# Kernel tuning notes

Hardware: AMD Instinct MI355X
Metric: run time of the kernel (lower is better)

## Reference

```python
import jax, jax.numpy as jnp
import numpy as np

# dims (match init_kwargs)
T, B, N, D_OB = 256, 32, 64, 4
D_MODEL = N * D_OB            # 256
D_PE = 16
D_T = D_MODEL + D_PE          # 272 transformer width
H = 8
DH = D_T // H                 # 34
L = 2
DFF = 1024
C = 2
MAX_LEN = T
F_IN = T * D_OB               # 1024, ObservationPropagation channels


def setup_inputs() -> dict:
    key = jax.random.key(0)
    ks = jax.random.split(key, 24)
    g = lambda k, shp: 0.02 * jax.random.normal(k, shp, dtype=jnp.float32)
    return {
        "x": jax.random.normal(ks[0], (T, B, N), dtype=jnp.float32),
        "times": jnp.sort(jax.random.uniform(ks[1], (T, B), dtype=jnp.float32) * MAX_LEN, axis=0),
        "lengths": jax.random.randint(ks[2], (B,), MAX_LEN // 2, MAX_LEN + 1),
        "R_u": g(ks[3], (1, N * D_OB)),
        "Wv1": g(ks[4], (F_IN, F_IN)), "bv1": g(ks[5], (F_IN,)),
        "Wv2": g(ks[6], (F_IN, F_IN)), "bv2": g(ks[7], (F_IN,)),
        "qkv_w": g(ks[8], (L, D_T, 3 * D_T)), "qkv_b": g(ks[9], (L, 3 * D_T)),
        "out_w": g(ks[10], (L, D_T, D_T)), "out_b": g(ks[11], (L, D_T)),
        "ln1_w": jnp.ones((L, D_T), jnp.float32), "ln1_b": jnp.zeros((L, D_T), jnp.float32),
        "ln2_w": jnp.ones((L, D_T), jnp.float32), "ln2_b": jnp.zeros((L, D_T), jnp.float32),
        "ffn_w1": g(ks[12], (L, D_T, DFF)), "ffn_b1": g(ks[13], (L, DFF)),
        "ffn_w2": g(ks[14], (L, DFF, D_T)), "ffn_b2": g(ks[15], (L, D_T)),
        "mlp_w1": g(ks[16], (D_T, D_T)), "mlp_b1": g(ks[17], (D_T,)),
        "mlp_w2": g(ks[18], (D_T, C)), "mlp_b2": g(ks[19], (C,)),
    }


def _pos_encode(times):
    # PositionalEncodingTF: timescales = max_len ** linspace(0,1,d_pe//2)
    scales = MAX_LEN ** np.linspace(0.0, 1.0, D_PE // 2)
    st = times[..., None] / jnp.asarray(scales, times.dtype)  # [T,B,8]
    return jnp.concatenate([jnp.sin(st), jnp.cos(st)], axis=-1)  # [T,B,16]


def _segment_softmax(w, seg, num_segments):
    m = jax.ops.segment_max(w, seg, num_segments=num_segments)
    e = jnp.exp(w - m[seg])
    s = jax.ops.segment_sum(e, seg, num_segments=num_segments)
    return e / s[seg]


def _ob_propagate(xn, src, tgt, edge_w, Wv, bv):
    """Batched ObservationPropagation (use_beta=False, decompose=False).
    xn: [B,N,F]; messages = relu(lin_value(x_src)) * softmax(edge_w per target);
    scatter-add at targets. Returns (out, pre-softmax alpha == edge_w)."""
    gamma = _segment_softmax(edge_w, tgt, N)              # [E]
    value = jax.nn.relu(xn @ Wv + bv)                     # [B,N,F] (linear commutes with gather)
    msg = value[:, src, :] * gamma[None, :, None]         # [B,E,F] -- dominant memory traffic
    out = jnp.zeros_like(xn).at[:, tgt, :].add(msg)       # segment-sum at target nodes
    return out, edge_w


def _ln(x, w, b):
    mu = jnp.mean(x, axis=-1, keepdims=True)
    var = jnp.mean((x - mu) ** 2, axis=-1, keepdims=True)
    return (x - mu) / jnp.sqrt(var + 1e-5) * w + b


def _encoder_layer(xt, key_pad, qkv_w, qkv_b, out_w, out_b, ln1_w, ln1_b, ln2_w, ln2_b, w1, b1, w2, b2):
    # xt: [T,B,D_T]; key_pad: [B,T] True = padded. Post-norm torch TransformerEncoderLayer, relu, no dropout.
    Tt, Bb, _ = xt.shape
    q, k, v = jnp.split(xt @ qkv_w + qkv_b, 3, axis=-1)
    to_h = lambda t: t.reshape(Tt, Bb, H, DH).transpose(1, 2, 0, 3)  # [B,H,T,dh]
    scores = jnp.einsum("bhqd,bhkd->bhqk", to_h(q), to_h(k)) / jnp.sqrt(jnp.asarray(DH, xt.dtype))
    scores = jnp.where(key_pad[:, None, None, :], -jnp.inf, scores)
    attn = jax.nn.softmax(scores, axis=-1)
    o = jnp.einsum("bhqk,bhkd->bhqd", attn, to_h(v)).transpose(2, 0, 1, 3).reshape(Tt, Bb, D_T)
    xt = _ln(xt + o @ out_w + out_b, ln1_w, ln1_b)
    ff = jax.nn.relu(xt @ w1 + b1) @ w2 + b2
    return _ln(xt + ff, ln2_w, ln2_b)


def _forward(x, times, lengths, R_u, Wv1, bv1, Wv2, bv2, qkv_w, qkv_b, out_w, out_b,
             ln1_w, ln1_b, ln2_w, ln2_b, ffn_w1, ffn_b1, ffn_w2, ffn_b2,
             mlp_w1, mlp_b1, mlp_w2, mlp_b2):
    Bb = x.shape[1]
    # observation embedding: repeat each sensor d_ob times, scale by R_u, relu
    h = jax.nn.relu(jnp.repeat(x, D_OB, axis=-1) * R_u)          # [T,B,N*d_ob]
    pe = _pos_encode(times)                                      # [T,B,16]
    key_pad = jnp.arange(T)[None, :] >= lengths[:, None]         # [B,T]
    # reshape to per-sensor node features: [B, N, T*d_ob]
    xn = h.reshape(T, Bb, N, D_OB).transpose(1, 2, 0, 3).reshape(Bb, N, F_IN)
    # dense all-pairs graph (global_structure = ones); torch.nonzero order is row-major
    src = jnp.repeat(jnp.arange(N), N)   # edge_index[0]
    tgt = jnp.tile(jnp.arange(N), N)     # edge_index[1] (aggregation index)
    ew = jnp.ones((N * N,), x.dtype)
    xn, ew2 = _ob_propagate(xn, src, tgt, ew, Wv1, bv1)
    xn, _ = _ob_propagate(xn, src, tgt, ew2, Wv2, bv2)
    out = xn.reshape(Bb, N, T, D_OB).transpose(2, 0, 1, 3).reshape(T, Bb, N * D_OB)
    out = jnp.concatenate([out, pe], axis=2)                     # [T,B,272]
    for l in range(L):
        out = _encoder_layer(out, key_pad, qkv_w[l], qkv_b[l], out_w[l], out_b[l],
                             ln1_w[l], ln1_b[l], ln2_w[l], ln2_b[l],
                             ffn_w1[l], ffn_b1[l], ffn_w2[l], ffn_b2[l])
    keep = (~key_pad).T[:, :, None].astype(out.dtype)            # [T,B,1]
    agg = jnp.sum(out * keep, axis=0) / (lengths[:, None].astype(out.dtype) + 1.0)
    hid = jax.nn.relu(agg @ mlp_w1 + mlp_b1)
    logits = hid @ mlp_w2 + mlp_b2
    return jax.nn.softmax(logits, axis=1)                        # [B,C]


def reference(x, times, lengths, R_u, Wv1, bv1, Wv2, bv2, qkv_w, qkv_b, out_w, out_b,
              ln1_w, ln1_b, ln2_w, ln2_b, ffn_w1, ffn_b1, ffn_w2, ffn_b2,
              mlp_w1, mlp_b1, mlp_w2, mlp_b2):
    return _forward(x, times, lengths, R_u, Wv1, bv1, Wv2, bv2, qkv_w, qkv_b, out_w, out_b,
                    ln1_w, ln1_b, ln2_w, ln2_b, ffn_w1, ffn_b1, ffn_w2, ffn_b2,
                    mlp_w1, mlp_b1, mlp_w2, mlp_b2)
```

## Files before the change

kernel.cpp:

```cpp
#include <hip/hip_runtime.h>
#include <math.h>

#define T_DIM 256
#define B_DIM 32
#define N_DIM 64
#define F_INF 1024
#define D_T 272
#define D_TP 288
#define H_DIM 8
#define DH_DIM 34
#define DFF_DIM 1024

typedef unsigned int uint;
typedef short bf16x8 __attribute__((ext_vector_type(8)));
typedef float f32x4 __attribute__((ext_vector_type(4)));

__device__ __forceinline__ ushort f2bf(float f) {
    uint u = __float_as_uint(f);
    uint r = (u + 0x7fffu + ((u >> 16) & 1u)) >> 16;
    return (ushort)r;
}
__device__ __forceinline__ float bf2f(ushort u) {
    return __uint_as_float(((uint)u) << 16);
}

__global__ void xn_kernel(const float* __restrict__ x, const float* __restrict__ Ru,
                          ushort* __restrict__ xn) {
    int idx = blockIdx.x * blockDim.x + threadIdx.x;
    if (idx >= B_DIM * N_DIM * F_INF) return;
    int f = idx & 1023;
    int bn = idx >> 10;
    int n = bn & 63;
    int b = bn >> 6;
    int t = f >> 2;
    int d = f & 3;
    float v = x[(t * B_DIM + b) * N_DIM + n] * Ru[(n << 2) + d];
    xn[idx] = f2bf(fmaxf(v, 0.0f));
}

struct WT {
    int tstart[11];
    const float* src[10];
    ushort* dst[10];
    int K[10];
    int N[10];
    int Kp[10];
    int ntn[10];
};
__global__ __launch_bounds__(256) void wconv_tiled(WT s) {
    int tile = blockIdx.x;
    int seg = 0;
    while (seg < 9 && tile >= s.tstart[seg + 1]) ++seg;
    int ti = tile - s.tstart[seg];
    int ntn = s.ntn[seg];
    int tk = ti / ntn, tn = ti - tk * ntn;
    int N = s.N[seg], Kp = s.Kp[seg];
    __shared__ float t[16][17];
    int ty = threadIdx.x >> 4, tx = threadIdx.x & 15;
    t[ty][tx] = s.src[seg][(size_t)(tk * 16 + ty) * N + tn * 16 + tx];
    __syncthreads();
    s.dst[seg][(size_t)(tn * 16 + ty) * Kp + tk * 16 + tx] = f2bf(t[tx][ty]);
}

template <int ACT, int OUT_MODE>
__global__ __launch_bounds__(256) void gemm_mfma(const ushort* __restrict__ A,
                                                 const ushort* __restrict__ Bt,
                                                 const float* __restrict__ bias,
                                                 void* __restrict__ Cout,
                                                 int M, int N, int K, int Kstride) {
    __shared__ ushort As[3][64 * 32];
    __shared__ ushort Bs[3][128 * 32];
    const int tid = threadIdx.x;
    const int m0 = (OUT_MODE == 3) ? 0 : blockIdx.y * 64;
    const int n0 = blockIdx.x * 128;
    if (OUT_MODE == 3) {
        A += (size_t)blockIdx.y * K;
        Bt += (size_t)blockIdx.y * K;
    }
    const int w = tid >> 6, lane = tid & 63;
    const int wr = w >> 1, wc = w & 1;
    const int lr = lane & 15, lk = lane >> 4;

    const int ns = K >> 5;

    const int ra = w * 16 + (lane >> 2);
    const int ca = (((lane & 3) ^ ((ra >> 1) & 3)) << 3);
    int gma = m0 + ra; if (gma > M - 1) gma = M - 1;
    const ushort* gA = &A[(size_t)gma * Kstride + ca];
    const int rb0 = w * 32 + (lane >> 2);
    const int cb0 = (((lane & 3) ^ ((rb0 >> 1) & 3)) << 3);
    const int rb1 = rb0 + 16;
    const int cb1 = (((lane & 3) ^ ((rb1 >> 1) & 3)) << 3);
    int gnb0 = n0 + rb0; if (gnb0 > N - 1) gnb0 = N - 1;
    int gnb1 = n0 + rb1; if (gnb1 > N - 1) gnb1 = N - 1;
    const ushort* gB0 = &Bt[(size_t)gnb0 * Kstride + cb0];
    const ushort* gB1 = &Bt[(size_t)gnb1 * Kstride + cb1];

    f32x4 acc[2][4];
#pragma unroll
    for (int i = 0; i < 2; ++i)
#pragma unroll
        for (int j = 0; j < 4; ++j) acc[i][j] = (f32x4){0.f, 0.f, 0.f, 0.f};

    auto stage = [&](int buf, int s) {
        const int k0 = s << 5;
        __builtin_amdgcn_global_load_lds(
            (const __attribute__((address_space(1))) void*)(gA + k0),
            (__attribute__((address_space(3))) void*)(&As[buf][w * 512]), 16, 0, 0);
        __builtin_amdgcn_global_load_lds(
            (const __attribute__((address_space(1))) void*)(gB0 + k0),
            (__attribute__((address_space(3))) void*)(&Bs[buf][w * 1024]), 16, 0, 0);
        __builtin_amdgcn_global_load_lds(
            (const __attribute__((address_space(1))) void*)(gB1 + k0),
            (__attribute__((address_space(3))) void*)(&Bs[buf][w * 1024 + 512]), 16, 0, 0);
    };

    stage(0, 0);
    stage(1, 1);
    asm volatile("s_waitcnt vmcnt(3)" ::: "memory");
    __builtin_amdgcn_sched_barrier(0);
    __builtin_amdgcn_s_barrier();
    __builtin_amdgcn_sched_barrier(0);

    int cur = 0;
    for (int s = 0; s < ns; ++s) {
        int stg = cur + 2; if (stg >= 3) stg -= 3;
        if (s + 2 < ns) stage(stg, s + 2);

        bf16x8 af[2], bf[4];
#pragma unroll
        for (int mt = 0; mt < 2; ++mt) {
            int row = wr * 32 + mt * 16 + lr;
            int ch = lk ^ ((row >> 1) & 3);
            af[mt] = *reinterpret_cast<const bf16x8*>(&As[cur][row * 32 + ch * 8]);
        }
#pragma unroll
        for (int nt = 0; nt < 4; ++nt) {
            int row = wc * 64 + nt * 16 + lr;
            int ch = lk ^ ((row >> 1) & 3);
            bf[nt] = *reinterpret_cast<const bf16x8*>(&Bs[cur][row * 32 + ch * 8]);
        }
        __builtin_amdgcn_s_setprio(1);
#pragma unroll
        for (int mt = 0; mt < 2; ++mt)
#pragma unroll
            for (int nt = 0; nt < 4; ++nt)
                acc[mt][nt] = __builtin_amdgcn_mfma_f32_16x16x32_bf16(
                    af[mt], bf[nt], acc[mt][nt], 0, 0, 0);
        __builtin_amdgcn_s_setprio(0);

        if (s + 1 < ns) {
            if (s + 2 < ns)
                asm volatile("s_waitcnt vmcnt(3)" ::: "memory");
            else
                asm volatile("s_waitcnt vmcnt(0)" ::: "memory");
            __builtin_amdgcn_sched_barrier(0);
            __builtin_amdgcn_s_barrier();
            __builtin_amdgcn_sched_barrier(0);
        }
        cur = (cur == 2) ? 0 : cur + 1;
    }

    if (OUT_MODE == 4) {
        __shared__ float red[2][128];
        float part[4];
#pragma unroll
        for (int nt = 0; nt < 4; ++nt) {
            int col = n0 + wc * 64 + nt * 16 + lr;
            float bv = bias[col];
            float s = 0.f;
#pragma unroll
            for (int mt = 0; mt < 2; ++mt)
#pragma unroll
                for (int r = 0; r < 4; ++r) s += fmaxf(acc[mt][nt][r] + bv, 0.f);
            s += __shfl_xor(s, 16);
            s += __shfl_xor(s, 32);
            part[nt] = s;
        }
        if (lk == 0) {
#pragma unroll
            for (int nt = 0; nt < 4; ++nt) red[wr][wc * 64 + nt * 16 + lr] = part[nt];
        }
        __syncthreads();
        if (tid < 128) {
            float tot = red[0][tid] + red[1][tid];
            ((ushort*)Cout)[(size_t)blockIdx.y * 1024 + n0 + tid] =
                f2bf(tot * (1.0f / 64.0f));
        }
        return;
    }

#pragma unroll
    for (int nt = 0; nt < 4; ++nt) {
        int col = n0 + wc * 64 + nt * 16 + lr;
        if (col >= N) continue;
        float bv = (OUT_MODE == 3) ? 0.f : bias[col];
        int g = 0, dcol = 0;
        if (OUT_MODE == 2) { g = col / 34; dcol = col - g * 34; }
#pragma unroll
        for (int mt = 0; mt < 2; ++mt) {
#pragma unroll
            for (int r = 0; r < 4; ++r) {
                int row = m0 + wr * 32 + mt * 16 + lk * 4 + r;
                if (row >= M) continue;
                float v = acc[mt][nt][r] + bv;
                if (ACT == 1) v = fmaxf(v, 0.0f);
                if (OUT_MODE == 0)
                    ((float*)Cout)[(size_t)row * N + col] = v;
                else if (OUT_MODE == 1)
                    ((ushort*)Cout)[(size_t)row * N + col] = f2bf(v);
                else if (OUT_MODE == 2)
                    ((ushort*)Cout)[(size_t)row * 960 + g * 40 + dcol] = f2bf(v);
                else
                    ((float*)Cout)[(size_t)(blockIdx.y * M + row) * N + col] = v;
            }
        }
    }
}

__global__ __launch_bounds__(256) void gemm_ln(const ushort* __restrict__ A,
                                               const ushort* __restrict__ Bt,
                                               const float* __restrict__ bias,
                                               const ushort* __restrict__ resid,
                                               const float* __restrict__ lnw,
                                               const float* __restrict__ lnb,
                                               ushort* __restrict__ Out,
                                               int K, int Kstride) {
    __shared__ ushort lds[21504];
    const int tid = threadIdx.x;
    const int m0 = blockIdx.x * 64;
    const int w = tid >> 6, lane = tid & 63;
    const int lr = lane & 15, lk = lane >> 4;
    const int ns = K >> 5;

    const int ra = w * 16 + (lane >> 2);
    const int ca = (((lane & 3) ^ ((ra >> 1) & 3)) << 3);
    const ushort* gA = &A[(size_t)(m0 + ra) * Kstride + ca];

    f32x4 acc[17];
#pragma unroll
    for (int t = 0; t < 17; ++t) acc[t] = (f32x4){0.f, 0.f, 0.f, 0.f};

    auto stage = [&](int buf, int s) {
        const int k0 = s << 5;
        __builtin_amdgcn_global_load_lds(
            (const __attribute__((address_space(1))) void*)(gA + k0),
            (__attribute__((address_space(3))) void*)(&lds[buf * 2048 + w * 512]),
            16, 0, 0);
        for (int c = w; c < 17; c += 4) {
            int row16 = c * 16 + (lane >> 2);
            int p8 = (((lane & 3) ^ ((row16 >> 1) & 3)) << 3);
            const ushort* src = &Bt[(size_t)row16 * Kstride + k0 + p8];
            __builtin_amdgcn_global_load_lds(
                (const __attribute__((address_space(1))) void*)src,
                (__attribute__((address_space(3))) void*)(&lds[4096 + buf * 8704 + c * 512]),
                16, 0, 0);
        }
    };

    stage(0, 0);
    asm volatile("s_waitcnt vmcnt(0)" ::: "memory");
    __builtin_amdgcn_sched_barrier(0);
    __builtin_amdgcn_s_barrier();
    __builtin_amdgcn_sched_barrier(0);

    int cur = 0;
    for (int s = 0; s < ns; ++s) {
        if (s + 1 < ns) stage(cur ^ 1, s + 1);

        bf16x8 af;
        {
            int row = w * 16 + lr;
            int ch = lk ^ ((row >> 1) & 3);
            af = *reinterpret_cast<const bf16x8*>(&lds[cur * 2048 + row * 32 + ch * 8]);
        }
        __builtin_amdgcn_s_setprio(1);
#pragma unroll
        for (int t = 0; t < 17; ++t) {
            int row = t * 16 + lr;
            int ch = lk ^ ((row >> 1) & 3);
            bf16x8 bf = *reinterpret_cast<const bf16x8*>(
                &lds[4096 + cur * 8704 + row * 32 + ch * 8]);
            acc[t] = __builtin_amdgcn_mfma_f32_16x16x32_bf16(af, bf, acc[t], 0, 0, 0);
        }
        __builtin_amdgcn_s_setprio(0);

        if (s + 1 < ns) {
            asm volatile("s_waitcnt vmcnt(0)" ::: "memory");
            __builtin_amdgcn_sched_barrier(0);
            __builtin_amdgcn_s_barrier();
            __builtin_amdgcn_sched_barrier(0);
        }
        cur ^= 1;
    }

    __syncthreads();
    for (int i = tid; i < 64 * 34; i += 256) {
        int row = i / 34, c8 = i - row * 34;
        *reinterpret_cast<uint4*>(&lds[row * 272 + c8 * 8]) =
            *reinterpret_cast<const uint4*>(&resid[(size_t)(m0 + row) * D_TP + c8 * 8]);
    }
    __syncthreads();

    float sum[4] = {0.f, 0.f, 0.f, 0.f}, sq[4] = {0.f, 0.f, 0.f, 0.f};
#pragma unroll
    for (int t = 0; t < 17; ++t) {
        int col = t * 16 + lr;
        float bv = bias[col];
#pragma unroll
        for (int r = 0; r < 4; ++r) {
            int row = w * 16 + lk * 4 + r;
            float v = acc[t][r] + bv + bf2f(lds[row * 272 + col]);
            acc[t][r] = v;
            sum[r] += v;
            sq[r] += v * v;
        }
    }
#pragma unroll
    for (int mask = 1; mask <= 8; mask <<= 1)
#pragma unroll
        for (int r = 0; r < 4; ++r) {
            sum[r] += __shfl_xor(sum[r], mask);
            sq[r] += __shfl_xor(sq[r], mask);
        }
    float mu[4], inv[4];
#pragma unroll
    for (int r = 0; r < 4; ++r) {
        mu[r] = sum[r] * (1.0f / D_T);
        float var = sq[r] * (1.0f / D_T) - mu[r] * mu[r];
        inv[r] = 1.0f / sqrtf(var + 1e-5f);
    }
#pragma unroll
    for (int t = 0; t < 17; ++t) {
        int col = t * 16 + lr;
        float wv = lnw[col], bb = lnb[col];
#pragma unroll
        for (int r = 0; r < 4; ++r) {
            int row = m0 + w * 16 + lk * 4 + r;
            Out[(size_t)row * D_TP + col] = f2bf((acc[t][r] - mu[r]) * inv[r] * wv + bb);
        }
    }
}

__global__ __launch_bounds__(256) void reduce_p2_kernel(const float* __restrict__ part,
                                                        const float* __restrict__ bv2,
                                                        float* __restrict__ out2) {
    int idx = blockIdx.x * 256 + threadIdx.x;
    if (idx >= B_DIM * F_INF) return;
    int g = idx & 1023;
    float s = bv2[g];
#pragma unroll
    for (int ks = 0; ks < 4; ++ks) s += part[(size_t)ks * B_DIM * F_INF + idx];
    out2[idx] = fmaxf(s, 0.f);
}

__global__ void seq_kernel(const float* __restrict__ out2, const float* __restrict__ times,
                           ushort* __restrict__ seq) {
    int idx = blockIdx.x * blockDim.x + threadIdx.x;
    if (idx >= T_DIM * B_DIM * D_TP) return;
    int c = idx % D_TP;
    int tb = idx / D_TP;
    float v;
    if (c < 256) {
        v = out2[(tb % B_DIM) * 1024 + ((tb / B_DIM) << 2) + (c & 3)];
    } else if (c < 272) {
        int s = c - 256;
        int sc = (s < 8) ? s : s - 8;
        float arg = times[tb] * exp2f(-8.0f * (float)sc * (1.0f / 7.0f));
        v = (s < 8) ? sinf(arg) : cosf(arg);
    } else {
        v = 0.f;
    }
    seq[idx] = f2bf(v);
}

struct PadPtrs {
    uint* wt[6];
    int nrows[6];
};
__global__ void init_pads_kernel(uint* __restrict__ qkvb, uint* __restrict__ x1,
                                 uint* __restrict__ attno, PadPtrs p) {
    const int TB = T_DIM * B_DIM;
    int idx = blockIdx.x * blockDim.x + threadIdx.x;
    if (idx < TB * 8) {
        int row = idx >> 3, q = idx & 7;
        x1[(size_t)row * 144 + 136 + q] = 0;
        attno[(size_t)row * 144 + 136 + q] = 0;
        return;
    }
    idx -= TB * 8;
    if (idx < TB * 72) {
        int row = idx / 72;
        int r = idx - row * 72;
        int g = r / 3, q = r - g * 3;
        qkvb[(size_t)row * 480 + g * 20 + 17 + q] = 0;
        return;
    }
    idx -= TB * 72;
#pragma unroll
    for (int sgi = 0; sgi < 6; ++sgi) {
        int cnt = p.nrows[sgi] * 8;
        if (idx < cnt) {
            int row = idx >> 3, q = idx & 7;
            p.wt[sgi][(size_t)row * 144 + 136 + q] = 0;
            return;
        }
        idx -= cnt;
    }
}

__global__ __launch_bounds__(256) void attn_mfma(const ushort* __restrict__ qkv,
                                                 const int* __restrict__ lengths,
                                                 ushort* __restrict__ attno) {
    const int b = blockIdx.x >> 3;
    const int h = blockIdx.x & 7;
    const int tid = threadIdx.x;
    const int w = tid >> 6, lane = tid & 63;
    const int lr = lane & 15, lk = lane >> 4;
    __shared__ ushort Ks[2][64 * 40];
    __shared__ ushort Vt[2][48 * 72];
    __shared__ ushort Ps[4][64 * 72];
    const int len = lengths[b];
    const float scale = 0.1714985851f;
    const bf16x8 zv = {0, 0, 0, 0, 0, 0, 0, 0};

    for (int i = tid; i < 2 * 8 * 72; i += 256) {
        int bb = i / 576;
        Vt[bb][40 * 72 + (i - bb * 576)] = 0;
    }

    const int srow0 = tid / 5, sch0 = tid - srow0 * 5;
    const int srow1 = (tid + 256) / 5, sch1 = (tid + 256) - srow1 * 5;
    const int sjp0 = (srow0 & 15) * 4 + (srow0 >> 4);
    const int sjp1 = (srow1 & 15) * 4 + (srow1 >> 4);
    const bool has1 = (tid < 64);
    bf16x8 kreg0, kreg1, vreg0, vreg1;

    auto LOADS = [&](int c) {
        const ushort* b0 = &qkv[(size_t)((c * 64 + srow0) * 32 + b) * 960 + h * 40];
        kreg0 = *reinterpret_cast<const bf16x8*>(b0 + 320 + sch0 * 8);
        vreg0 = *reinterpret_cast<const bf16x8*>(b0 + 640 + sch0 * 8);
        if (has1) {
            const ushort* b1 = &qkv[(size_t)((c * 64 + srow1) * 32 + b) * 960 + h * 40];
            kreg1 = *reinterpret_cast<const bf16x8*>(b1 + 320 + sch1 * 8);
            vreg1 = *reinterpret_cast<const bf16x8*>(b1 + 640 + sch1 * 8);
        }
    };
    auto WRITES = [&](int buf) {
        *reinterpret_cast<bf16x8*>(&Ks[buf][srow0 * 40 + sch0 * 8]) = kreg0;
#pragma unroll
        for (int e = 0; e < 8; ++e) Vt[buf][(sch0 * 8 + e) * 72 + sjp0] = (ushort)vreg0[e];
        if (has1) {
            *reinterpret_cast<bf16x8*>(&Ks[buf][srow1 * 40 + sch1 * 8]) = kreg1;
#pragma unroll
            for (int e = 0; e < 8; ++e) Vt[buf][(sch1 * 8 + e) * 72 + sjp1] = (ushort)vreg1[e];
        }
    };

    bf16x8 qf0[4], qf1[4];
#pragma unroll
    for (int it = 0; it < 4; ++it) {
        int t = w * 64 + it * 16 + lr;
        const ushort* qrow = &qkv[(size_t)(t * 32 + b) * 960 + h * 40];
        qf0[it] = *reinterpret_cast<const bf16x8*>(qrow + lk * 8);
        qf1[it] = (lk == 0) ? *reinterpret_cast<const bf16x8*>(qrow + 32) : zv;
    }

    f32x4 oacc[4][3];
#pragma unroll
    for (int it = 0; it < 4; ++it)
#pragma unroll
        for (int dt = 0; dt < 3; ++dt) oacc[it][dt] = (f32x4){0.f, 0.f, 0.f, 0.f};
    float m[4][4], l[4][4];
#pragma unroll
    for (int it = 0; it < 4; ++it)
#pragma unroll
        for (int r = 0; r < 4; ++r) { m[it][r] = -1e30f; l[it][r] = 0.f; }

    const int nchunks = (len + 63) >> 6;
    LOADS(0);
    WRITES(0);
    __syncthreads();

    int cur = 0;
    for (int c = 0; c < nchunks; ++c) {
        const bool pre = (c + 1 < nchunks);
        if (pre) LOADS(c + 1);

        bf16x8 kf0[4], kf1[4];
#pragma unroll
        for (int jt = 0; jt < 4; ++jt) {
            int j = jt * 16 + lr;
            kf0[jt] = *reinterpret_cast<const bf16x8*>(&Ks[cur][j * 40 + lk * 8]);
            kf1[jt] = (lk == 0) ? *reinterpret_cast<const bf16x8*>(&Ks[cur][j * 40 + 32]) : zv;
        }

        const bool tail = (c * 64 + 64 > len);
#pragma unroll
        for (int it = 0; it < 4; ++it) {
            f32x4 sacc[4];
#pragma unroll
            for (int jt = 0; jt < 4; ++jt) sacc[jt] = (f32x4){0.f, 0.f, 0.f, 0.f};
            __builtin_amdgcn_s_setprio(1);
#pragma unroll
            for (int jt = 0; jt < 4; ++jt) {
                sacc[jt] = __builtin_amdgcn_mfma_f32_16x16x32_bf16(qf0[it], kf0[jt],
                                                                   sacc[jt], 0, 0, 0);
                sacc[jt] = __builtin_amdgcn_mfma_f32_16x16x32_bf16(qf1[it], kf1[jt],
                                                                   sacc[jt], 0, 0, 0);
            }
            __builtin_amdgcn_s_setprio(0);
            float cm[4] = {-1e30f, -1e30f, -1e30f, -1e30f};
#pragma unroll
            for (int jt = 0; jt < 4; ++jt) {
                bool dead = tail && (c * 64 + jt * 16 + lr >= len);
#pragma unroll
                for (int r = 0; r < 4; ++r) {
                    float sv = dead ? -1e30f : sacc[jt][r];
                    sacc[jt][r] = sv;
                    cm[r] = fmaxf(cm[r], sv);
                }
            }
#pragma unroll
            for (int mask = 1; mask <= 8; mask <<= 1)
#pragma unroll
                for (int r = 0; r < 4; ++r) cm[r] = fmaxf(cm[r], __shfl_xor(cm[r], mask));
#pragma unroll
            for (int r = 0; r < 4; ++r) {
                float mn = fmaxf(m[it][r], cm[r]);
                float corr = __expf((m[it][r] - mn) * scale);
                m[it][r] = mn;
                l[it][r] *= corr;
#pragma unroll
                for (int dt = 0; dt < 3; ++dt) oacc[it][dt][r] *= corr;
            }
            float ls[4] = {0.f, 0.f, 0.f, 0.f};
#pragma unroll
            for (int jt = 0; jt < 4; ++jt)
#pragma unroll
                for (int r = 0; r < 4; ++r) {
                    float e = __expf((sacc[jt][r] - m[it][r]) * scale);
                    sacc[jt][r] = e;
                    ls[r] += e;
                }
#pragma unroll
            for (int mask = 1; mask <= 8; mask <<= 1)
#pragma unroll
                for (int r = 0; r < 4; ++r) ls[r] += __shfl_xor(ls[r], mask);
#pragma unroll
            for (int r = 0; r < 4; ++r) l[it][r] += ls[r];
#pragma unroll
            for (int r = 0; r < 4; ++r) {
                int i = it * 16 + lk * 4 + r;
                uint u0 = (uint)f2bf(sacc[0][r]) | ((uint)f2bf(sacc[1][r]) << 16);
                uint u1 = (uint)f2bf(sacc[2][r]) | ((uint)f2bf(sacc[3][r]) << 16);
                uint2 pk = make_uint2(u0, u1);
                *reinterpret_cast<uint2*>(&Ps[w][i * 72 + lr * 4]) = pk;
            }
        }

        bf16x8 vf[3][2], pf[4][2];
#pragma unroll
        for (int dt = 0; dt < 3; ++dt)
#pragma unroll
            for (int ks = 0; ks < 2; ++ks)
                vf[dt][ks] = *reinterpret_cast<const bf16x8*>(
                    &Vt[cur][(dt * 16 + lr) * 72 + ks * 32 + lk * 8]);
#pragma unroll
        for (int it = 0; it < 4; ++it)
#pragma unroll
            for (int ks = 0; ks < 2; ++ks)
                pf[it][ks] = *reinterpret_cast<const bf16x8*>(
                    &Ps[w][(it * 16 + lr) * 72 + ks * 32 + lk * 8]);
        __builtin_amdgcn_s_setprio(1);
#pragma unroll
        for (int it = 0; it < 4; ++it)
#pragma unroll
            for (int dt = 0; dt < 3; ++dt)
#pragma unroll
                for (int ks = 0; ks < 2; ++ks)
                    oacc[it][dt] = __builtin_amdgcn_mfma_f32_16x16x32_bf16(
                        pf[it][ks], vf[dt][ks], oacc[it][dt], 0, 0, 0);
        __builtin_amdgcn_s_setprio(0);

        if (pre) WRITES(cur ^ 1);
        __syncthreads();
        cur ^= 1;
    }

#pragma unroll
    for (int it = 0; it < 4; ++it)
#pragma unroll
        for (int r = 0; r < 4; ++r) {
            float inv = 1.0f / l[it][r];
            int t = w * 64 + it * 16 + lk * 4 + r;
            ushort* orow = &attno[(size_t)(t * 32 + b) * D_TP + h * 34];
#pragma unroll
            for (int dt = 0; dt < 3; ++dt) {
                int d = dt * 16 + lr;
                if (d < 34) orow[d] = f2bf(oacc[it][dt][r] * inv);
            }
        }
}

__global__ __launch_bounds__(256) void pool_partial(const ushort* __restrict__ seq,
                                                    const int* __restrict__ lengths,
                                                    float* __restrict__ partial) {
    const int chunk = blockIdx.x;
    const int b = blockIdx.y;
    const int tid = threadIdx.x;
    if (tid >= 136) return;
    const int len = lengths[b];
    float s0 = 0.f, s1 = 0.f;
    int t0 = chunk * 32;
    int tmax = len - t0;
    if (tmax > 32) tmax = 32;
#pragma unroll 4
    for (int r = 0; r < tmax; ++r) {
        uint u = *reinterpret_cast<const uint*>(
            &seq[(size_t)((t0 + r) * B_DIM + b) * D_TP + tid * 2]);
        s0 += __uint_as_float(u << 16);
        s1 += __uint_as_float(u & 0xffff0000u);
    }
    float* p = &partial[(size_t)(chunk * B_DIM + b) * D_T + tid * 2];
    p[0] = s0;
    p[1] = s1;
}

__global__ __launch_bounds__(256) void head_kernel(const float* __restrict__ partial,
                                                   const int* __restrict__ lengths,
                                                   const float* __restrict__ w1,
                                                   const float* __restrict__ b1,
                                                   const float* __restrict__ w2,
                                                   const float* __restrict__ b2,
                                                   float* __restrict__ out) {
    const int b = blockIdx.x;
    const int tid = threadIdx.x;
    const int len = lengths[b];
    __shared__ float agg_s[D_T];
    __shared__ float hid[D_T];
    float inv = 1.0f / (float)(len + 1);
    for (int c = tid; c < D_T; c += 256) {
        float s = 0.f;
#pragma unroll
        for (int ch = 0; ch < 8; ++ch)
            s += partial[(size_t)(ch * B_DIM + b) * D_T + c];
        agg_s[c] = s * inv;
    }
    __syncthreads();
    for (int j = tid; j < D_T; j += 256) {
        float acc = b1[j];
        for (int k = 0; k < D_T; ++k) acc += agg_s[k] * w1[k * D_T + j];
        hid[j] = fmaxf(acc, 0.f);
    }
    __syncthreads();
    if (tid < 64) {
        float l0 = 0.f, l1 = 0.f;
        for (int k = tid; k < D_T; k += 64) {
            float hv = hid[k];
            l0 += hv * w2[k * 2 + 0];
            l1 += hv * w2[k * 2 + 1];
        }
#pragma unroll
        for (int off = 32; off; off >>= 1) {
            l0 += __shfl_down(l0, off);
            l1 += __shfl_down(l1, off);
        }
        if (tid == 0) {
            l0 += b2[0];
            l1 += b2[1];
            float mx = fmaxf(l0, l1);
            float e0 = expf(l0 - mx), e1 = expf(l1 - mx);
            float nrm = 1.0f / (e0 + e1);
            out[b * 2 + 0] = e0 * nrm;
            out[b * 2 + 1] = e1 * nrm;
        }
    }
}

extern "C" void kernel_launch(void* const* d_in, const int* in_sizes, int n_in,
                              void* d_out, int out_size, void* d_ws, size_t ws_size,
                              hipStream_t stream) {
    const float* x      = (const float*)d_in[0];
    const float* times  = (const float*)d_in[1];
    const int*   lens   = (const int*)d_in[2];
    const float* R_u    = (const float*)d_in[3];
    const float* Wv1    = (const float*)d_in[4];
    const float* bv1    = (const float*)d_in[5];
    const float* Wv2    = (const float*)d_in[6];
    const float* bv2    = (const float*)d_in[7];
    const float* qkv_w  = (const float*)d_in[8];
    const float* qkv_b  = (const float*)d_in[9];
    const float* out_w  = (const float*)d_in[10];
    const float* out_b  = (const float*)d_in[11];
    const float* ln1_w  = (const float*)d_in[12];
    const float* ln1_b  = (const float*)d_in[13];
    const float* ln2_w  = (const float*)d_in[14];
    const float* ln2_b  = (const float*)d_in[15];
    const float* ffn_w1 = (const float*)d_in[16];
    const float* ffn_b1 = (const float*)d_in[17];
    const float* ffn_w2 = (const float*)d_in[18];
    const float* ffn_b2 = (const float*)d_in[19];
    const float* mlp_w1 = (const float*)d_in[20];
    const float* mlp_b1 = (const float*)d_in[21];
    const float* mlp_w2 = (const float*)d_in[22];
    const float* mlp_b2 = (const float*)d_in[23];
    float* outp = (float*)d_out;

    char* base = (char*)d_ws;
    size_t used = 0;
    auto alloc = [&](size_t bytes) -> char* {
        char* p = base + used;
        used += (bytes + 255) & ~(size_t)255;
        return p;
    };
    const int TB = T_DIM * B_DIM;

    ushort* xn    = (ushort*)alloc((size_t)2048 * 1024 * 2);
    ushort* s1    = (ushort*)alloc((size_t)32 * 1024 * 2);
    float*  p2p   = (float*) alloc((size_t)4 * 32 * 1024 * 4);
    float*  out2  = (float*) alloc((size_t)32 * 1024 * 4);
    ushort* seq   = (ushort*)alloc((size_t)TB * D_TP * 2);
    ushort* qkvb  = (ushort*)alloc((size_t)TB * 960 * 2);
    ushort* attno = (ushort*)alloc((size_t)TB * D_TP * 2);
    ushort* x1    = (ushort*)alloc((size_t)TB * D_TP * 2);
    ushort* h1    = (ushort*)alloc((size_t)TB * DFF_DIM * 2);
    float*  ppart = (float*) alloc((size_t)8 * B_DIM * D_T * 4);
    ushort* wv1t  = (ushort*)alloc((size_t)1024 * 1024 * 2);
    ushort* wv2t  = (ushort*)alloc((size_t)1024 * 1024 * 2);
    ushort* qkvwt[2]; ushort* outwt[2]; ushort* f1wt[2]; ushort* f2wt[2];
    for (int l = 0; l < 2; ++l) {
        qkvwt[l] = (ushort*)alloc((size_t)816 * D_TP * 2);
        outwt[l] = (ushort*)alloc((size_t)272 * D_TP * 2);
        f1wt[l]  = (ushort*)alloc((size_t)1024 * D_TP * 2);
        f2wt[l]  = (ushort*)alloc((size_t)272 * 1024 * 2);
    }
    if (used > ws_size) return;

    {
        WT segs;
        const float* srcs[10] = {Wv1, Wv2,
                                 qkv_w, out_w, ffn_w1, ffn_w2,
                                 qkv_w + (size_t)272 * 816, out_w + (size_t)272 * 272,
                                 ffn_w1 + (size_t)272 * 1024, ffn_w2 + (size_t)1024 * 272};
        ushort* dsts[10] = {wv1t, wv2t, qkvwt[0], outwt[0], f1wt[0], f2wt[0],
                            qkvwt[1], outwt[1], f1wt[1], f2wt[1]};
        int Ksz[10] = {1024, 1024, 272, 272, 272, 1024, 272, 272, 272, 1024};
        int Nsz[10] = {1024, 1024, 816, 272, 1024, 272, 816, 272, 1024, 272};
        int Kpd[10] = {1024, 1024, D_TP, D_TP, D_TP, 1024, D_TP, D_TP, D_TP, 1024};
        int acc = 0;
        for (int i = 0; i < 10; ++i) {
            segs.tstart[i] = acc;
            segs.src[i] = srcs[i];
            segs.dst[i] = dsts[i];
            segs.K[i] = Ksz[i];
            segs.N[i] = Nsz[i];
            segs.Kp[i] = Kpd[i];
            segs.ntn[i] = Nsz[i] / 16;
            acc += (Ksz[i] / 16) * (Nsz[i] / 16);
        }
        segs.tstart[10] = acc;
        wconv_tiled<<<acc, 256, 0, stream>>>(segs);
    }

    {
        PadPtrs pp;
        pp.wt[0] = (uint*)qkvwt[0]; pp.nrows[0] = 816;
        pp.wt[1] = (uint*)qkvwt[1]; pp.nrows[1] = 816;
        pp.wt[2] = (uint*)outwt[0]; pp.nrows[2] = 272;
        pp.wt[3] = (uint*)outwt[1]; pp.nrows[3] = 272;
        pp.wt[4] = (uint*)f1wt[0];  pp.nrows[4] = 1024;
        pp.wt[5] = (uint*)f1wt[1];  pp.nrows[5] = 1024;
        int n = TB * 8 + TB * 72 + (816 + 816 + 272 + 272 + 1024 + 1024) * 8;
        init_pads_kernel<<<(n + 255) / 256, 256, 0, stream>>>((uint*)qkvb, (uint*)x1,
                                                              (uint*)attno, pp);
    }

    {
        int n = B_DIM * N_DIM * F_INF;
        xn_kernel<<<(n + 255) / 256, 256, 0, stream>>>(x, R_u, xn);
    }

    gemm_mfma<1, 4><<<dim3(8, 32), 256, 0, stream>>>(xn, wv1t, bv1, s1,
                                                     2048, 1024, 1024, 1024);
    gemm_mfma<0, 3><<<dim3(8, 4), 256, 0, stream>>>(s1, wv2t, nullptr, p2p,
                                                    32, 1024, 256, 1024);
    reduce_p2_kernel<<<128, 256, 0, stream>>>(p2p, bv2, out2);

    {
        int n = TB * D_TP;
        seq_kernel<<<(n + 255) / 256, 256, 0, stream>>>(out2, times, seq);
    }

    for (int l = 0; l < 2; ++l) {
        const float* qb  = qkv_b + (size_t)l * 816;
        const float* ob  = out_b + (size_t)l * D_T;
        const float* l1w = ln1_w + (size_t)l * D_T;
        const float* l1b = ln1_b + (size_t)l * D_T;
        const float* l2w = ln2_w + (size_t)l * D_T;
        const float* l2b = ln2_b + (size_t)l * D_T;
        const float* f1b = ffn_b1 + (size_t)l * DFF_DIM;
        const float* f2b = ffn_b2 + (size_t)l * D_T;

        gemm_mfma<0, 2><<<dim3(7, 128), 256, 0, stream>>>(seq, qkvwt[l], qb, qkvb,
                                                          TB, 816, D_TP, D_TP);
        attn_mfma<<<B_DIM * H_DIM, 256, 0, stream>>>(qkvb, lens, attno);
        gemm_ln<<<128, 256, 0, stream>>>(attno, outwt[l], ob, seq, l1w, l1b, x1,
                                         D_TP, D_TP);
        gemm_mfma<1, 1><<<dim3(8, 128), 256, 0, stream>>>(x1, f1wt[l], f1b, h1,
                                                          TB, DFF_DIM, D_TP, D_TP);
        gemm_ln<<<128, 256, 0, stream>>>(h1, f2wt[l], f2b, x1, l2w, l2b, seq,
                                         1024, 1024);
    }

    pool_partial<<<dim3(8, B_DIM), 256, 0, stream>>>(seq, lens, ppart);
    head_kernel<<<B_DIM, 256, 0, stream>>>(ppart, lens, mlp_w1, mlp_b1,
                                           mlp_w2, mlp_b2, outp);
}
```

Before: 287.7 us.

## Triple-buffer gemm_ln loads and merge xn and pad-init kernels

The LN-fused GEMM moves from double to triple buffering in LDS, so stage s+2 is prefetched while stage s is computed. The wait counts are per-wave, since wave 0 issues one extra B-load. This hides more global-load latency, but LDS use per block grows from about 43KB to about 64KB, which can lower occupancy. Separately, the xn computation and the pad-zeroing kernel are merged into one launch to remove a kernel launch.

```diff
diff --git a/kernel.cpp b/kernel.cpp
--- a/kernel.cpp
+++ b/kernel.cpp
@@ -22,20 +22,6 @@
 }
 __device__ __forceinline__ float bf2f(ushort u) {
     return __uint_as_float(((uint)u) << 16);
-}
-
-__global__ void xn_kernel(const float* __restrict__ x, const float* __restrict__ Ru,
-                          ushort* __restrict__ xn) {
-    int idx = blockIdx.x * blockDim.x + threadIdx.x;
-    if (idx >= B_DIM * N_DIM * F_INF) return;
-    int f = idx & 1023;
-    int bn = idx >> 10;
-    int n = bn & 63;
-    int b = bn >> 6;
-    int t = f >> 2;
-    int d = f & 3;
-    float v = x[(t * B_DIM + b) * N_DIM + n] * Ru[(n << 2) + d];
-    xn[idx] = f2bf(fmaxf(v, 0.0f));
 }
 
 struct WT {
@@ -62,6 +48,55 @@
     s.dst[seg][(size_t)(tn * 16 + ty) * Kp + tk * 16 + tx] = f2bf(t[tx][ty]);
 }
 
+struct PadPtrs {
+    uint* wt[6];
+    int nrows[6];
+};
+__global__ void init_kernel(const float* __restrict__ x, const float* __restrict__ Ru,
+                            ushort* __restrict__ xn, uint* __restrict__ qkvb,
+                            uint* __restrict__ x1, uint* __restrict__ attno, PadPtrs p) {
+    const int TB = T_DIM * B_DIM;
+    const int NXN = B_DIM * N_DIM * F_INF;
+    int idx = blockIdx.x * blockDim.x + threadIdx.x;
+    if (idx < NXN) {
+        int f = idx & 1023;
+        int bn = idx >> 10;
+        int n = bn & 63;
+        int b = bn >> 6;
+        int t = f >> 2;
+        int d = f & 3;
+        float v = x[(t * B_DIM + b) * N_DIM + n] * Ru[(n << 2) + d];
+        xn[idx] = f2bf(fmaxf(v, 0.0f));
+        return;
+    }
+    idx -= NXN;
+    if (idx < TB * 8) {
+        int row = idx >> 3, q = idx & 7;
+        x1[(size_t)row * 144 + 136 + q] = 0;
+        attno[(size_t)row * 144 + 136 + q] = 0;
+        return;
+    }
+    idx -= TB * 8;
+    if (idx < TB * 72) {
+        int row = idx / 72;
+        int r = idx - row * 72;
+        int g = r / 3, q = r - g * 3;
+        qkvb[(size_t)row * 480 + g * 20 + 17 + q] = 0;
+        return;
+    }
+    idx -= TB * 72;
+#pragma unroll
+    for (int sgi = 0; sgi < 6; ++sgi) {
+        int cnt = p.nrows[sgi] * 8;
+        if (idx < cnt) {
+            int row = idx >> 3, q = idx & 7;
+            p.wt[sgi][(size_t)row * 144 + 136 + q] = 0;
+            return;
+        }
+        idx -= cnt;
+    }
+}
+
 template <int ACT, int OUT_MODE>
 __global__ __launch_bounds__(256) void gemm_mfma(const ushort* __restrict__ A,
                                                  const ushort* __restrict__ Bt,
@@ -226,7 +261,7 @@
                                                const float* __restrict__ lnb,
                                                ushort* __restrict__ Out,
                                                int K, int Kstride) {
-    __shared__ ushort lds[21504];
+    __shared__ ushort lds[32256];
     const int tid = threadIdx.x;
     const int m0 = blockIdx.x * 64;
     const int w = tid >> 6, lane = tid & 63;
@@ -253,20 +288,25 @@
             const ushort* src = &Bt[(size_t)row16 * Kstride + k0 + p8];
             __builtin_amdgcn_global_load_lds(
                 (const __attribute__((address_space(1))) void*)src,
-                (__attribute__((address_space(3))) void*)(&lds[4096 + buf * 8704 + c * 512]),
+                (__attribute__((address_space(3))) void*)(&lds[6144 + buf * 8704 + c * 512]),
                 16, 0, 0);
         }
     };
 
     stage(0, 0);
-    asm volatile("s_waitcnt vmcnt(0)" ::: "memory");
+    stage(1, 1);
+    if (w == 0)
+        asm volatile("s_waitcnt vmcnt(6)" ::: "memory");
+    else
+        asm volatile("s_waitcnt vmcnt(5)" ::: "memory");
     __builtin_amdgcn_sched_barrier(0);
     __builtin_amdgcn_s_barrier();
     __builtin_amdgcn_sched_barrier(0);
 
     int cur = 0;
     for (int s = 0; s < ns; ++s) {
-        if (s + 1 < ns) stage(cur ^ 1, s + 1);
+        int stg = cur + 2; if (stg >= 3) stg -= 3;
+        if (s + 2 < ns) stage(stg, s + 2);
 
         bf16x8 af;
         {
@@ -280,18 +320,25 @@
             int row = t * 16 + lr;
             int ch = lk ^ ((row >> 1) & 3);
             bf16x8 bf = *reinterpret_cast<const bf16x8*>(
-                &lds[4096 + cur * 8704 + row * 32 + ch * 8]);
+                &lds[6144 + cur * 8704 + row * 32 + ch * 8]);
             acc[t] = __builtin_amdgcn_mfma_f32_16x16x32_bf16(af, bf, acc[t], 0, 0, 0);
         }
         __builtin_amdgcn_s_setprio(0);
 
         if (s + 1 < ns) {
-            asm volatile("s_waitcnt vmcnt(0)" ::: "memory");
+            if (s + 2 < ns) {
+                if (w == 0)
+                    asm volatile("s_waitcnt vmcnt(6)" ::: "memory");
+                else
+                    asm volatile("s_waitcnt vmcnt(5)" ::: "memory");
+            } else {
+                asm volatile("s_waitcnt vmcnt(0)" ::: "memory");
+            }
             __builtin_amdgcn_sched_barrier(0);
             __builtin_amdgcn_s_barrier();
             __builtin_amdgcn_sched_barrier(0);
         }
-        cur ^= 1;
+        cur = (cur == 2) ? 0 : cur + 1;
     }
 
     __syncthreads();
@@ -372,41 +419,6 @@
         v = 0.f;
     }
     seq[idx] = f2bf(v);
-}
-
-struct PadPtrs {
-    uint* wt[6];
-    int nrows[6];
-};
-__global__ void init_pads_kernel(uint* __restrict__ qkvb, uint* __restrict__ x1,
-                                 uint* __restrict__ attno, PadPtrs p) {
-    const int TB = T_DIM * B_DIM;
-    int idx = blockIdx.x * blockDim.x + threadIdx.x;
-    if (idx < TB * 8) {
-        int row = idx >> 3, q = idx & 7;
-        x1[(size_t)row * 144 + 136 + q] = 0;
-        attno[(size_t)row * 144 + 136 + q] = 0;
-        return;
-    }
-    idx -= TB * 8;
-    if (idx < TB * 72) {
-        int row = idx / 72;
-        int r = idx - row * 72;
-        int g = r / 3, q = r - g * 3;
-        qkvb[(size_t)row * 480 + g * 20 + 17 + q] = 0;
-        return;
-    }
-    idx -= TB * 72;
-#pragma unroll
-    for (int sgi = 0; sgi < 6; ++sgi) {
-        int cnt = p.nrows[sgi] * 8;
-        if (idx < cnt) {
-            int row = idx >> 3, q = idx & 7;
-            p.wt[sgi][(size_t)row * 144 + 136 + q] = 0;
-            return;
-        }
-        idx -= cnt;
-    }
 }
 
 __global__ __launch_bounds__(256) void attn_mfma(const ushort* __restrict__ qkv,
@@ -771,14 +783,10 @@
         pp.wt[3] = (uint*)outwt[1]; pp.nrows[3] = 272;
         pp.wt[4] = (uint*)f1wt[0];  pp.nrows[4] = 1024;
         pp.wt[5] = (uint*)f1wt[1];  pp.nrows[5] = 1024;
-        int n = TB * 8 + TB * 72 + (816 + 816 + 272 + 272 + 1024 + 1024) * 8;
-        init_pads_kernel<<<(n + 255) / 256, 256, 0, stream>>>((uint*)qkvb, (uint*)x1,
-                                                              (uint*)attno, pp);
-    }
-
-    {
-        int n = B_DIM * N_DIM * F_INF;
-        xn_kernel<<<(n + 255) / 256, 256, 0, stream>>>(x, R_u, xn);
+        int n = B_DIM * N_DIM * F_INF + TB * 8 + TB * 72 +
+                (816 + 816 + 272 + 272 + 1024 + 1024) * 8;
+        init_kernel<<<(n + 255) / 256, 256, 0, stream>>>(x, R_u, xn, (uint*)qkvb,
+                                                         (uint*)x1, (uint*)attno, pp);
     }
 
     gemm_mfma<1, 4><<<dim3(8, 32), 256, 0, stream>>>(xn, wv1t, bv1, s1,
```

New measurement: 288.1 us. No clear change (+0.2%).
